# Performance work log

Hardware: AMD Instinct MI355X
Metric: run time of the kernel (lower is better)

The kernel has to match this reference:

```python
import jax, jax.numpy as jnp
import numpy as np

B, S, I, H, O = 64, 2048, 256, 512, 256

def setup_inputs() -> dict:
    key = jax.random.key(0)
    k_x, k_wxh, k_whh, k_why = jax.random.split(key, 4)
    return {
        "x": jax.random.normal(k_x, (B, S, I), dtype=jnp.float32),
        "Wxh": jax.random.normal(k_wxh, (I, H), dtype=jnp.float32),
        "Whh": jax.random.normal(k_whh, (H, H), dtype=jnp.float32),
        "Why": jax.random.normal(k_why, (H, O), dtype=jnp.float32),
        "bias_h": jnp.zeros((1, H), dtype=jnp.float32),
        "bias_y": jnp.zeros((1, O), dtype=jnp.float32),
    }

def reference(x, Wxh, Whh, Why, bias_h, bias_y):
    # x: [B, S, I]. Precompute input projections for all timesteps in one GEMM.
    xw = jnp.einsum("bsi,ih->bsh", x, Wxh) + bias_h  # [B, S, H]
    h0 = jnp.zeros((x.shape[0], Whh.shape[0]), dtype=x.dtype)

    def step(h, xw_t):
        h_new = jnp.tanh(xw_t + h @ Whh)
        return h_new, None

    h_last, _ = jax.lax.scan(step, h0, jnp.swapaxes(xw, 0, 1))  # scan over time
    return h_last @ Why + bias_y  # [B, O]
```

## Files before the change

### kernel.cpp

```cpp
#include <hip/hip_runtime.h>
#include <stdint.h>

#define Bn 64
#define Sn 2048
#define In 256
#define Hn 512
#define On 256
#define TT 16
#define CH 32


__device__ __forceinline__ float xla_tanh(float x) {
    const float ax = __builtin_fabsf(x);
    float xc = fmaxf(-7.99881172180175781f, fminf(7.99881172180175781f, x));
    const float x2 = xc * xc;
    float p = fmaf(x2, -2.76076847742355e-16f, 2.00018790482477e-13f);
    p = fmaf(x2, p, -8.60467152213735e-11f);
    p = fmaf(x2, p, 5.12229709037114e-08f);
    p = fmaf(x2, p, 1.48572235717979e-05f);
    p = fmaf(x2, p, 6.37261928875436e-04f);
    p = fmaf(x2, p, 4.89352455891786e-03f);
    p = xc * p;
    float q = fmaf(x2, 1.19825839466702e-06f, 1.18534705686654e-04f);
    q = fmaf(x2, q, 2.26843463243900e-03f);
    q = fmaf(x2, q, 4.89352518554385e-03f);
    return ax < 0.0004f ? x : p / q;
}

__global__ __launch_bounds__(512) void xw_gemm(const float* __restrict__ x,
                                               const float* __restrict__ Wxh,
                                               const float* __restrict__ bias_h,
                                               float* __restrict__ xw) {
    const int b = blockIdx.x >> 7;
    const int t0 = (blockIdx.x & 127) * TT;
    const int j = threadIdx.x;
    __shared__ float xl[TT][In];

    const float4* xsrc = (const float4*)(x + ((size_t)b * Sn + t0) * In);
    float4* xdst = (float4*)&xl[0][0];
    for (int u = j; u < TT * In / 4; u += 512) xdst[u] = xsrc[u];
    __syncthreads();

    float acc[TT];
#pragma unroll
    for (int m = 0; m < TT; ++m) acc[m] = 0.f;

    for (int i = 0; i < In; i += 4) {
        const float w0 = Wxh[(size_t)(i + 0) * Hn + j];
        const float w1 = Wxh[(size_t)(i + 1) * Hn + j];
        const float w2 = Wxh[(size_t)(i + 2) * Hn + j];
        const float w3 = Wxh[(size_t)(i + 3) * Hn + j];
#pragma unroll
        for (int m = 0; m < TT; ++m) {
            const float4 xv = *(const float4*)&xl[m][i];
            float a = acc[m];
            a = fmaf(xv.x, w0, a);
            a = fmaf(xv.y, w1, a);
            a = fmaf(xv.z, w2, a);
            a = fmaf(xv.w, w3, a);
            acc[m] = a;
        }
    }
    const float bh = bias_h[j];
#pragma unroll
    for (int m = 0; m < TT; ++m)
        xw[((size_t)b * Sn + t0 + m) * Hn + j] = acc[m] + bh;
}

#define CHUNKW(WP, HP4, CUR, NXT, C)                                          \
    {                                                                         \
        const int kpre_ = (((C) + 2) & 15) * CH;                              \
        _Pragma("unroll") for (int u_ = 0; u_ < CH; ++u_)                     \
            NXT[u_] = (WP)[(size_t)(kpre_ + u_) * 256];                       \
        _Pragma("unroll") for (int u_ = 0; u_ < CH; u_ += 4) {                \
            const float4 hv_ = (HP4)[((C) * CH + u_) >> 2];                   \
            a0 = fmaf(hv_.x, CUR[u_ + 0].x, a0); a1 = fmaf(hv_.x, CUR[u_ + 0].y, a1); \
            a0 = fmaf(hv_.y, CUR[u_ + 1].x, a0); a1 = fmaf(hv_.y, CUR[u_ + 1].y, a1); \
            a0 = fmaf(hv_.z, CUR[u_ + 2].x, a0); a1 = fmaf(hv_.z, CUR[u_ + 2].y, a1); \
            a0 = fmaf(hv_.w, CUR[u_ + 3].x, a0); a1 = fmaf(hv_.w, CUR[u_ + 3].y, a1); \
        }                                                                     \
    }

#define CHUNKL(WP, HP4, CUR, NXT, C, N, A0, A1)                               \
    {                                                                         \
        if ((C) + 2 < (N)) {                                                  \
            _Pragma("unroll") for (int u_ = 0; u_ < CH; ++u_)                 \
                NXT[u_] = (WP)[(size_t)(((C) + 2) * CH + u_) * 256];          \
        }                                                                     \
        _Pragma("unroll") for (int u_ = 0; u_ < CH; u_ += 4) {                \
            const float4 hv_ = (HP4)[((C) * CH + u_) >> 2];                   \
            A0 = fmaf(hv_.x, CUR[u_ + 0].x, A0); A1 = fmaf(hv_.x, CUR[u_ + 0].y, A1); \
            A0 = fmaf(hv_.y, CUR[u_ + 1].x, A0); A1 = fmaf(hv_.y, CUR[u_ + 1].y, A1); \
            A0 = fmaf(hv_.z, CUR[u_ + 2].x, A0); A1 = fmaf(hv_.z, CUR[u_ + 2].y, A1); \
            A0 = fmaf(hv_.w, CUR[u_ + 3].x, A0); A1 = fmaf(hv_.w, CUR[u_ + 3].y, A1); \
        }                                                                     \
    }

template <bool PRE>
__global__ __launch_bounds__(256, 1) void rnn_stream(
        const float* __restrict__ Whh,
        const float* __restrict__ xw_or_x,
        const float* __restrict__ Wxh,
        const float* __restrict__ bias_h,
        float* __restrict__ hlast) {
    const int b = blockIdx.x;
    const int tid = threadIdx.x;
    const int j0 = tid * 2;

    __shared__ float hs[2][Hn];
    __shared__ float xr[2][In];

    hs[0][j0] = 0.f;
    hs[0][j0 + 1] = 0.f;
    float bh0 = 0.f, bh1 = 0.f;
    if constexpr (!PRE) {
        xr[0][tid] = xw_or_x[(size_t)b * Sn * In + tid];
        bh0 = bias_h[j0];
        bh1 = bias_h[j0 + 1];
    }
    __syncthreads();

    const float2* wp = (const float2*)Whh + tid;

    float2 wa[CH], wb[CH], wc[CH], wd[CH];
    if constexpr (PRE) {
#pragma unroll
        for (int u = 0; u < CH; ++u) {
            wa[u] = wp[(size_t)(0 * CH + u) * 256];
            wb[u] = wp[(size_t)(1 * CH + u) * 256];
        }
    }

    float hn0 = 0.f, hn1 = 0.f;

    for (int t = 0; t < Sn; ++t) {
        const int p = t & 1;
        const float4* h4 = (const float4*)&hs[p][0];
        float a0 = 0.f, a1 = 0.f;
        float xw0, xw1;

        if constexpr (PRE) {
            const float2 xv = *(const float2*)(xw_or_x + ((size_t)b * Sn + t) * Hn + j0);
            for (int cc = 0; cc < 16; cc += 4) {
                CHUNKW(wp, h4, wa, wc, cc + 0);
                CHUNKW(wp, h4, wb, wd, cc + 1);
                CHUNKW(wp, h4, wc, wa, cc + 2);
                CHUNKW(wp, h4, wd, wb, cc + 3);
            }
            xw0 = xv.x;
            xw1 = xv.y;
        } else {
            float xnext = 0.f;
            if (t + 1 < Sn)
                xnext = xw_or_x[((size_t)b * Sn + t + 1) * In + tid];

            const float2* wxp = (const float2*)Wxh + tid;
            const float4* x4 = (const float4*)&xr[p][0];
            float xa0 = 0.f, xa1 = 0.f;
#pragma unroll
            for (int u = 0; u < CH; ++u) {
                wa[u] = wxp[(size_t)u * 256];
                wb[u] = wxp[(size_t)(CH + u) * 256];
            }
            CHUNKL(wxp, x4, wa, wc, 0, 8, xa0, xa1);
            CHUNKL(wxp, x4, wb, wd, 1, 8, xa0, xa1);
            CHUNKL(wxp, x4, wc, wa, 2, 8, xa0, xa1);
            CHUNKL(wxp, x4, wd, wb, 3, 8, xa0, xa1);
            CHUNKL(wxp, x4, wa, wc, 4, 8, xa0, xa1);
            CHUNKL(wxp, x4, wb, wd, 5, 8, xa0, xa1);
            CHUNKL(wxp, x4, wc, wa, 6, 8, xa0, xa1);
            CHUNKL(wxp, x4, wd, wb, 7, 8, xa0, xa1);
            xw0 = xa0 + bh0;
            xw1 = xa1 + bh1;

#pragma unroll
            for (int u = 0; u < CH; ++u) {
                wa[u] = wp[(size_t)u * 256];
                wb[u] = wp[(size_t)(CH + u) * 256];
            }
            for (int cc = 0; cc < 16; cc += 4) {
                CHUNKL(wp, h4, wa, wc, cc + 0, 16, a0, a1);
                CHUNKL(wp, h4, wb, wd, cc + 1, 16, a0, a1);
                CHUNKL(wp, h4, wc, wa, cc + 2, 16, a0, a1);
                CHUNKL(wp, h4, wd, wb, cc + 3, 16, a0, a1);
            }
            if (t + 1 < Sn) xr[1 - p][tid] = xnext;
        }

        const float u0 = xw0 + a0;
        const float u1 = xw1 + a1;
        hn0 = xla_tanh(u0);
        hn1 = xla_tanh(u1);
        hs[1 - p][j0] = hn0;
        hs[1 - p][j0 + 1] = hn1;
        __syncthreads();
    }

    hlast[(size_t)b * Hn + j0] = hn0;
    hlast[(size_t)b * Hn + j0 + 1] = hn1;
}

__global__ __launch_bounds__(256) void out_gemm(const float* __restrict__ hlast,
                                                const float* __restrict__ Why,
                                                const float* __restrict__ bias_y,
                                                float* __restrict__ y) {
    const int b = blockIdx.x, o = threadIdx.x;
    __shared__ float hs[Hn];
    hs[o] = hlast[(size_t)b * Hn + o];
    hs[o + 256] = hlast[(size_t)b * Hn + o + 256];
    __syncthreads();
    float acc = 0.0f;
#pragma unroll 8
    for (int k = 0; k < Hn; ++k)
        acc = fmaf(hs[k], Why[(size_t)k * On + o], acc);
    y[(size_t)b * On + o] = acc + bias_y[o];
}

extern "C" void kernel_launch(void* const* d_in, const int* in_sizes, int n_in,
                              void* d_out, int out_size, void* d_ws, size_t ws_size,
                              hipStream_t stream) {
    const float *x = nullptr, *Wxh = nullptr, *Whh = nullptr, *Why = nullptr,
                *bias_h = nullptr, *bias_y = nullptr;
    for (int i = 0; i < n_in; ++i) {
        const float* p = (const float*)d_in[i];
        const int sz = in_sizes[i];
        if (sz == Bn * Sn * In) x = p;
        else if (sz == Hn * Hn) Whh = p;
        else if (sz == In * Hn) { if (!Wxh) Wxh = p; else Why = p; }
        else if (sz == Hn) bias_h = p;
        else if (sz == On) bias_y = p;
    }
    float* y = (float*)d_out;

    char* ws = (char*)d_ws;
    float* hlast = (float*)ws;
    const size_t hlast_bytes = (size_t)Bn * Hn * sizeof(float);
    float* xw = (float*)(ws + hlast_bytes);
    const size_t xw_bytes = (size_t)Bn * Sn * Hn * sizeof(float);

    if (ws_size >= hlast_bytes + xw_bytes) {
        xw_gemm<<<dim3(Bn * (Sn / TT)), dim3(512), 0, stream>>>(x, Wxh, bias_h, xw);
        rnn_stream<true><<<dim3(Bn), dim3(256), 0, stream>>>(Whh, xw, nullptr,
                                                             nullptr, hlast);
    } else {
        rnn_stream<false><<<dim3(Bn), dim3(256), 0, stream>>>(Whh, x, Wxh,
                                                              bias_h, hlast);
    }
    out_gemm<<<dim3(Bn), dim3(On), 0, stream>>>(hlast, Why, bias_y, y);
}
```

Measured before the change: 30.00 ms.

## Split Whh across registers, LDS and streamed loads in 512-thread scan kernel

Replaces the precomputed-xw recurrence kernel with a 512-thread-per-batch kernel where each thread owns one hidden unit. The first 128 rows of Whh are held in registers, the next 64 rows in shared memory, and the remaining 320 rows are streamed from global/L2 with a 4-deep rotating prefetch. This is meant to cut the per-step global weight traffic that bounded the old kernel, at the cost of heavy register pressure and possible spilling. The fallback path is kept but renamed and de-templated.

```diff
diff --git a/kernel.cpp b/kernel.cpp
--- a/kernel.cpp
+++ b/kernel.cpp
@@ -8,6 +8,12 @@
 #define On 256
 #define TT 16
 #define CH 32
+
+#define RK 128
+#define LK 64
+#define SK (Hn - RK - LK)
+#define SC 16
+#define NCH (SK / SC)
 
 
 __device__ __forceinline__ float xla_tanh(float x) {
@@ -67,19 +73,91 @@
         xw[((size_t)b * Sn + t0 + m) * Hn + j] = acc[m] + bh;
 }
 
-#define CHUNKW(WP, HP4, CUR, NXT, C)                                          \
+__global__ __launch_bounds__(512, 2) void rnn_scan512(const float* __restrict__ Whh,
+                                                      const float* __restrict__ xw,
+                                                      float* __restrict__ hlast) {
+    const int b = blockIdx.x;
+    const int tid = threadIdx.x;
+
+    __shared__ float hs[2][Hn];
+    __shared__ float wl[LK][Hn];
+
+    float wr[RK];
+#pragma unroll
+    for (int k = 0; k < RK; ++k) wr[k] = Whh[(size_t)k * Hn + tid];
+
+    {
+        const float4* src = (const float4*)(Whh + (size_t)RK * Hn);
+        float4* dst = (float4*)&wl[0][0];
+#pragma unroll
+        for (int u = 0; u < (LK * Hn / 4) / 512; ++u)
+            dst[u * 512 + tid] = src[u * 512 + tid];
+    }
+    hs[0][tid] = 0.f;
+    __syncthreads();
+
+    const float* wsrc = Whh + (size_t)(RK + LK) * Hn + tid;
+
+    float s0[SC], s1[SC], s2[SC], s3[SC];
+#define ISSUE(BUF, C)                                                         \
     {                                                                         \
-        const int kpre_ = (((C) + 2) & 15) * CH;                              \
-        _Pragma("unroll") for (int u_ = 0; u_ < CH; ++u_)                     \
-            NXT[u_] = (WP)[(size_t)(kpre_ + u_) * 256];                       \
-        _Pragma("unroll") for (int u_ = 0; u_ < CH; u_ += 4) {                \
-            const float4 hv_ = (HP4)[((C) * CH + u_) >> 2];                   \
-            a0 = fmaf(hv_.x, CUR[u_ + 0].x, a0); a1 = fmaf(hv_.x, CUR[u_ + 0].y, a1); \
-            a0 = fmaf(hv_.y, CUR[u_ + 1].x, a0); a1 = fmaf(hv_.y, CUR[u_ + 1].y, a1); \
-            a0 = fmaf(hv_.z, CUR[u_ + 2].x, a0); a1 = fmaf(hv_.z, CUR[u_ + 2].y, a1); \
-            a0 = fmaf(hv_.w, CUR[u_ + 3].x, a0); a1 = fmaf(hv_.w, CUR[u_ + 3].y, a1); \
+        const float* p_ = wsrc + (size_t)(C) * SC * Hn;                       \
+        _Pragma("unroll") for (int u_ = 0; u_ < SC; ++u_)                     \
+            BUF[u_] = p_[(size_t)u_ * Hn];                                    \
+    }
+
+    ISSUE(s0, 0) ISSUE(s1, 1) ISSUE(s2, 2) ISSUE(s3, 3)
+
+    float hn = 0.f;
+    for (int t = 0; t < Sn; ++t) {
+        const int p = t & 1;
+        const float xwv = xw[((size_t)b * Sn + t) * Hn + tid];
+        const float4* h4 = (const float4*)&hs[p][0];
+        float acc = 0.f;
+
+#pragma unroll
+        for (int q = 0; q < RK / 4; ++q) {
+            const float4 hv = h4[q];
+            acc = fmaf(hv.x, wr[4 * q + 0], acc);
+            acc = fmaf(hv.y, wr[4 * q + 1], acc);
+            acc = fmaf(hv.z, wr[4 * q + 2], acc);
+            acc = fmaf(hv.w, wr[4 * q + 3], acc);
+        }
+#pragma unroll
+        for (int q = 0; q < LK / 4; ++q) {
+            const float4 hv = h4[RK / 4 + q];
+            acc = fmaf(hv.x, wl[4 * q + 0][tid], acc);
+            acc = fmaf(hv.y, wl[4 * q + 1][tid], acc);
+            acc = fmaf(hv.z, wl[4 * q + 2][tid], acc);
+            acc = fmaf(hv.w, wl[4 * q + 3][tid], acc);
+        }
+#define SCHUNK(BUF, C)                                                        \
+    {                                                                         \
+        _Pragma("unroll") for (int u_ = 0; u_ < SC; u_ += 4) {                \
+            const float4 hv_ = h4[(RK + LK) / 4 + ((C) * SC + u_) / 4];       \
+            acc = fmaf(hv_.x, BUF[u_ + 0], acc);                              \
+            acc = fmaf(hv_.y, BUF[u_ + 1], acc);                              \
+            acc = fmaf(hv_.z, BUF[u_ + 2], acc);                              \
+            acc = fmaf(hv_.w, BUF[u_ + 3], acc);                              \
         }                                                                     \
-    }
+        ISSUE(BUF, ((C) + 4) % NCH)                                           \
+    }
+
+#pragma unroll
+        for (int cc = 0; cc < NCH; cc += 4) {
+            SCHUNK(s0, cc + 0)
+            SCHUNK(s1, cc + 1)
+            SCHUNK(s2, cc + 2)
+            SCHUNK(s3, cc + 3)
+        }
+
+        const float u = xwv + acc;
+        hn = xla_tanh(u);
+        hs[1 - p][tid] = hn;
+        __syncthreads();
+    }
+    hlast[(size_t)b * Hn + tid] = hn;
+}
 
 #define CHUNKL(WP, HP4, CUR, NXT, C, N, A0, A1)                               \
     {                                                                         \
@@ -96,12 +174,9 @@
         }                                                                     \
     }
 
-template <bool PRE>
-__global__ __launch_bounds__(256, 1) void rnn_stream(
-        const float* __restrict__ Whh,
-        const float* __restrict__ xw_or_x,
-        const float* __restrict__ Wxh,
-        const float* __restrict__ bias_h,
+__global__ __launch_bounds__(256, 1) void rnn_fallback(
+        const float* __restrict__ Whh, const float* __restrict__ x,
+        const float* __restrict__ Wxh, const float* __restrict__ bias_h,
         float* __restrict__ hlast) {
     const int b = blockIdx.x;
     const int tid = threadIdx.x;
@@ -112,80 +187,54 @@
 
     hs[0][j0] = 0.f;
     hs[0][j0 + 1] = 0.f;
-    float bh0 = 0.f, bh1 = 0.f;
-    if constexpr (!PRE) {
-        xr[0][tid] = xw_or_x[(size_t)b * Sn * In + tid];
-        bh0 = bias_h[j0];
-        bh1 = bias_h[j0 + 1];
-    }
+    const float bh0 = bias_h[j0];
+    const float bh1 = bias_h[j0 + 1];
+    xr[0][tid] = x[(size_t)b * Sn * In + tid];
     __syncthreads();
 
     const float2* wp = (const float2*)Whh + tid;
-
     float2 wa[CH], wb[CH], wc[CH], wd[CH];
-    if constexpr (PRE) {
-#pragma unroll
-        for (int u = 0; u < CH; ++u) {
-            wa[u] = wp[(size_t)(0 * CH + u) * 256];
-            wb[u] = wp[(size_t)(1 * CH + u) * 256];
-        }
-    }
-
     float hn0 = 0.f, hn1 = 0.f;
 
     for (int t = 0; t < Sn; ++t) {
         const int p = t & 1;
         const float4* h4 = (const float4*)&hs[p][0];
         float a0 = 0.f, a1 = 0.f;
-        float xw0, xw1;
-
-        if constexpr (PRE) {
-            const float2 xv = *(const float2*)(xw_or_x + ((size_t)b * Sn + t) * Hn + j0);
-            for (int cc = 0; cc < 16; cc += 4) {
-                CHUNKW(wp, h4, wa, wc, cc + 0);
-                CHUNKW(wp, h4, wb, wd, cc + 1);
-                CHUNKW(wp, h4, wc, wa, cc + 2);
-                CHUNKW(wp, h4, wd, wb, cc + 3);
-            }
-            xw0 = xv.x;
-            xw1 = xv.y;
-        } else {
-            float xnext = 0.f;
-            if (t + 1 < Sn)
-                xnext = xw_or_x[((size_t)b * Sn + t + 1) * In + tid];
-
-            const float2* wxp = (const float2*)Wxh + tid;
-            const float4* x4 = (const float4*)&xr[p][0];
-            float xa0 = 0.f, xa1 = 0.f;
-#pragma unroll
-            for (int u = 0; u < CH; ++u) {
-                wa[u] = wxp[(size_t)u * 256];
-                wb[u] = wxp[(size_t)(CH + u) * 256];
-            }
-            CHUNKL(wxp, x4, wa, wc, 0, 8, xa0, xa1);
-            CHUNKL(wxp, x4, wb, wd, 1, 8, xa0, xa1);
-            CHUNKL(wxp, x4, wc, wa, 2, 8, xa0, xa1);
-            CHUNKL(wxp, x4, wd, wb, 3, 8, xa0, xa1);
-            CHUNKL(wxp, x4, wa, wc, 4, 8, xa0, xa1);
-            CHUNKL(wxp, x4, wb, wd, 5, 8, xa0, xa1);
-            CHUNKL(wxp, x4, wc, wa, 6, 8, xa0, xa1);
-            CHUNKL(wxp, x4, wd, wb, 7, 8, xa0, xa1);
-            xw0 = xa0 + bh0;
-            xw1 = xa1 + bh1;
-
-#pragma unroll
-            for (int u = 0; u < CH; ++u) {
-                wa[u] = wp[(size_t)u * 256];
-                wb[u] = wp[(size_t)(CH + u) * 256];
-            }
-            for (int cc = 0; cc < 16; cc += 4) {
-                CHUNKL(wp, h4, wa, wc, cc + 0, 16, a0, a1);
-                CHUNKL(wp, h4, wb, wd, cc + 1, 16, a0, a1);
-                CHUNKL(wp, h4, wc, wa, cc + 2, 16, a0, a1);
-                CHUNKL(wp, h4, wd, wb, cc + 3, 16, a0, a1);
-            }
-            if (t + 1 < Sn) xr[1 - p][tid] = xnext;
-        }
+
+        float xnext = 0.f;
+        if (t + 1 < Sn) xnext = x[((size_t)b * Sn + t + 1) * In + tid];
+
+        const float2* wxp = (const float2*)Wxh + tid;
+        const float4* x4 = (const float4*)&xr[p][0];
+        float xa0 = 0.f, xa1 = 0.f;
+#pragma unroll
+        for (int u = 0; u < CH; ++u) {
+            wa[u] = wxp[(size_t)u * 256];
+            wb[u] = wxp[(size_t)(CH + u) * 256];
+        }
+        CHUNKL(wxp, x4, wa, wc, 0, 8, xa0, xa1);
+        CHUNKL(wxp, x4, wb, wd, 1, 8, xa0, xa1);
+        CHUNKL(wxp, x4, wc, wa, 2, 8, xa0, xa1);
+        CHUNKL(wxp, x4, wd, wb, 3, 8, xa0, xa1);
+        CHUNKL(wxp, x4, wa, wc, 4, 8, xa0, xa1);
+        CHUNKL(wxp, x4, wb, wd, 5, 8, xa0, xa1);
+        CHUNKL(wxp, x4, wc, wa, 6, 8, xa0, xa1);
+        CHUNKL(wxp, x4, wd, wb, 7, 8, xa0, xa1);
+        const float xw0 = xa0 + bh0;
+        const float xw1 = xa1 + bh1;
+
+#pragma unroll
+        for (int u = 0; u < CH; ++u) {
+            wa[u] = wp[(size_t)u * 256];
+            wb[u] = wp[(size_t)(CH + u) * 256];
+        }
+        for (int cc = 0; cc < 16; cc += 4) {
+            CHUNKL(wp, h4, wa, wc, cc + 0, 16, a0, a1);
+            CHUNKL(wp, h4, wb, wd, cc + 1, 16, a0, a1);
+            CHUNKL(wp, h4, wc, wa, cc + 2, 16, a0, a1);
+            CHUNKL(wp, h4, wd, wb, cc + 3, 16, a0, a1);
+        }
+        if (t + 1 < Sn) xr[1 - p][tid] = xnext;
 
         const float u0 = xw0 + a0;
         const float u1 = xw1 + a1;
@@ -195,7 +244,6 @@
         hs[1 - p][j0 + 1] = hn1;
         __syncthreads();
     }
-
     hlast[(size_t)b * Hn + j0] = hn0;
     hlast[(size_t)b * Hn + j0 + 1] = hn1;
 }
@@ -240,11 +288,9 @@
 
     if (ws_size >= hlast_bytes + xw_bytes) {
         xw_gemm<<<dim3(Bn * (Sn / TT)), dim3(512), 0, stream>>>(x, Wxh, bias_h, xw);
-        rnn_stream<true><<<dim3(Bn), dim3(256), 0, stream>>>(Whh, xw, nullptr,
-                                                             nullptr, hlast);
+        rnn_scan512<<<dim3(Bn), dim3(512), 0, stream>>>(Whh, xw, hlast);
     } else {
-        rnn_stream<false><<<dim3(Bn), dim3(256), 0, stream>>>(Whh, x, Wxh,
-                                                              bias_h, hlast);
+        rnn_fallback<<<dim3(Bn), dim3(256), 0, stream>>>(Whh, x, Wxh, bias_h, hlast);
     }
     out_gemm<<<dim3(Bn), dim3(On), 0, stream>>>(hlast, Why, bias_y, y);
 }
```

New measurement: 39.80 ms. +32.6%, slower.
